# Kernel tuning notes

Hardware: AMD Instinct MI355X
Metric: run time of the kernel (lower is better)

## Reference

```python
import jax, jax.numpy as jnp
import numpy as np

B, H, W = 2, 32, 128
HW = H * W
N, C = 4096, 64
KQ, KN = 32, 16          # nsample_q, nsample
DIST = 10.0              # neighbor distance threshold
NEG = -1e10


def _knn(q, p, k):
    # q: (B,M,3), p: (B,N,3) -> idx (B,M,k), sqdist (B,M,k)
    sqd = jnp.sum((q[:, :, None, :] - p[:, None, :, :]) ** 2, axis=-1)
    neg, idx = jax.lax.top_k(-sqd, k)
    return idx, -neg


def _gather(p, idx):
    # p: (B,N,C), idx: (B,M,K) -> (B,M,K,C)
    return jax.vmap(lambda a, i: a[i])(p, idx)


def _norm_feat(x):
    # per-point channel normalization, torch.std default is unbiased (ddof=1)
    m = jnp.mean(x, axis=-1, keepdims=True)
    s = jnp.clip(jnp.std(x, axis=-1, keepdims=True, ddof=1), 1e-12)
    return (x - m) / s


def _conv(x, w, b, g, e):
    # 1x1 conv + BatchNorm (track_running_stats=False -> batch stats) + LeakyReLU(0.1)
    y = jnp.einsum('bnkc,cd->bnkd', x, w) + b
    mu = y.mean(axis=(0, 1, 2), keepdims=True)
    var = y.var(axis=(0, 1, 2), keepdims=True)
    y = (y - mu) * jax.lax.rsqrt(var + 1e-5) * g + e
    return jnp.where(y > 0, y, 0.1 * y)


def setup_inputs() -> dict:
    key = jax.random.key(0)
    ks = jax.random.split(key, 20)
    inp = {
        'xyz_proj_raw': jax.random.normal(ks[0], (B, H, W, 3), jnp.float32),
        'warped_xyz': jax.random.normal(ks[1], (B, HW, 3), jnp.float32),
        'warped_points': jax.random.normal(ks[2], (B, HW, C), jnp.float32),
        'idx_n2': jax.random.randint(ks[3], (B, HW, 2), 0, W),
        'f2_xyz': jax.random.normal(ks[4], (B, N, 3), jnp.float32),
        'f2_points': jax.random.normal(ks[5], (B, N, C), jnp.float32),
        'lidar_z': jax.random.uniform(ks[6], (B, HW, 1), jnp.float32),
    }
    shapes = {
        'm1w0': (70, 128), 'm1w1': (128, 64), 'piw': (6, 64),
        'm2w0': (128, 64), 'm2w1': (64, 64), 'pcw': (10, 64),
        'm3w0': (192, 64), 'm3w1': (64, 64),
    }
    i = 7
    for name, shp in shapes.items():
        inp[name] = jax.random.normal(ks[i], shp, jnp.float32) * 0.05
        i += 1
        pre = name[:-2] if name[-2] == 'w' else name[:-1]
        suf = name[-1] if name[-2] == 'w' else ''
        cout = shp[1]
        inp[pre + 'b' + suf] = jnp.zeros((cout,), jnp.float32)
        inp[pre + 'g' + suf] = jnp.ones((cout,), jnp.float32)
        inp[pre + 'e' + suf] = jnp.zeros((cout,), jnp.float32)
    return inp


def reference(xyz_proj_raw, warped_xyz, warped_points, idx_n2, f2_xyz, f2_points, lidar_z,
              m1w0, m1b0, m1g0, m1e0, m1w1, m1b1, m1g1, m1e1,
              piw, pib, pig, pie,
              m2w0, m2b0, m2g0, m2e0, m2w1, m2b1, m2g1, m2e1,
              pcw, pcb, pcg, pce,
              m3w0, m3b0, m3g0, m3e0, m3w1, m3b1, m3g1, m3e1):
    # ---- stage 1: cross kNN grouping into image features ----
    idx_q, _ = _knn(warped_xyz, f2_xyz, KQ)
    qi_xyz = _gather(f2_xyz, idx_q)          # (B,HW,KQ,3)
    qi_pts = _gather(f2_points, idx_q)       # (B,HW,KQ,C)

    wxyz = warped_xyz * lidar_z              # (B,HW,3)
    pi_xyz_exp = jnp.broadcast_to(wxyz[:, :, None, :], (B, HW, KQ, 3))
    pi_pts_exp = jnp.broadcast_to(warped_points[:, :, None, :], (B, HW, KQ, C))
    pi_xyz_diff_concat = jnp.concatenate([pi_xyz_exp, qi_xyz], axis=3)  # (B,HW,KQ,6)

    pi_feat_diff = _norm_feat(pi_pts_exp) * _norm_feat(qi_pts)          # correlation
    feat = jnp.concatenate([pi_xyz_diff_concat, pi_feat_diff], axis=3)  # (B,HW,KQ,70)

    feat = _conv(feat, m1w0, m1b0, m1g0, m1e0)
    feat = _conv(feat, m1w1, m1b1, m1g1, m1e1)                          # (B,HW,KQ,64)
    pi_enc = _conv(pi_xyz_diff_concat, piw, pib, pig, pie)              # (B,HW,KQ,64)

    pi_cat = jnp.concatenate([pi_enc, feat], axis=3)
    pi_cat = _conv(pi_cat, m2w0, m2b0, m2g0, m2e0)
    pi_cat = _conv(pi_cat, m2w1, m2b1, m2g1, m2e1)
    WQ = jax.nn.softmax(pi_cat, axis=2)
    pi_feat1 = jnp.sum(WQ * feat, axis=2)                               # (B,HW,64)

    # ---- stage 2: self kNN (use_trans=False -> raw projected xyz), thresholded validity ----
    xyz_pr = xyz_proj_raw.reshape(B, HW, 3)
    idx2, sqd2 = _knn(xyz_pr, xyz_pr, KN)
    valid = (sqd2 < DIST * DIST).astype(pi_feat1.dtype)[..., None]      # (B,HW,KN,1)

    pc_xyz_g = _gather(wxyz, idx2)                                      # (B,HW,KN,3)
    pc_pts_g = _gather(pi_feat1, idx2)                                  # (B,HW,KN,64)
    pc_xyz_new = jnp.broadcast_to(wxyz[:, :, None, :], (B, HW, KN, 3))
    pc_pts_new = jnp.broadcast_to(warped_points[:, :, None, :], (B, HW, KN, C))

    pc_diff = pc_xyz_g - pc_xyz_new
    pc_euc = jnp.sqrt(jnp.sum(pc_diff * pc_diff, axis=3, keepdims=True) + 1e-20)
    pc_xyz_cat = jnp.concatenate([pc_xyz_new, pc_xyz_g, pc_diff, pc_euc], axis=3)  # 10ch

    pc_enc = _conv(pc_xyz_cat, pcw, pcb, pcg, pce)
    pc_cat = jnp.concatenate([pc_enc, pc_pts_new, pc_pts_g], axis=-1)   # (B,HW,KN,192)
    pc_cat = _conv(pc_cat, m3w0, m3b0, m3g0, m3e0)
    pc_cat = _conv(pc_cat, m3w1, m3b1, m3g1, m3e1)

    pc_cat = pc_cat * valid + NEG * (1.0 - valid)
    WP = jax.nn.softmax(pc_cat, axis=2)
    out = jnp.sum(WP * pc_pts_g, axis=2)                                # (B,HW,64)
    return out.reshape(B, H, W, -1)
```

## Files before the change

### kernel.cpp

```cpp
#include <hip/hip_runtime.h>
#include <math.h>

constexpr int Bn  = 2;
constexpr int HWn = 4096;
constexpr int Nn  = 4096;
constexpr int KQn = 32;
constexpr int KNn = 16;
constexpr float INV_R1 = 1.0f/262144.0f;
constexpr float INV_R2 = 1.0f/131072.0f;

typedef _Float16 f16x8 __attribute__((ext_vector_type(8)));
typedef float    f32x4 __attribute__((ext_vector_type(4)));

__device__ __forceinline__ float wred64(float v){
  #pragma unroll
  for (int m = 32; m > 0; m >>= 1) v += __shfl_xor(v, m, 64);
  return v;
}
__device__ __forceinline__ float leakyf(float v){ return v > 0.f ? v : 0.1f*v; }

__device__ __forceinline__ void bn_param(const float* st, int c, float inv_n,
                                         const float* g, const float* e,
                                         float& sc, float& sh){
  float mu  = st[c]*inv_n;
  float var = st[128+c]*inv_n - mu*mu;
  float s   = g[c]*rsqrtf(var + 1e-5f);
  sc = s; sh = e[c] - mu*s;
}

__device__ __forceinline__ void build_x70(int row,
    const float* __restrict__ wxyz, const float* __restrict__ f2_xyz,
    const float* __restrict__ normW, const float* __restrict__ normF2,
    const int* __restrict__ idxq, float* x){
  int p = row >> 5;
  int b = p >> 12;
  int idx = idxq[row];
  const float* wx = wxyz + (size_t)p*3;
  const float* fx = f2_xyz + ((size_t)b*Nn + idx)*3;
  x[0]=wx[0]; x[1]=wx[1]; x[2]=wx[2];
  x[3]=fx[0]; x[4]=fx[1]; x[5]=fx[2];
  const float4* nw = (const float4*)(normW  + (size_t)p*64);
  const float4* nf = (const float4*)(normF2 + ((size_t)b*Nn + idx)*64);
  #pragma unroll
  for (int c=0;c<16;c++){
    float4 a = nw[c], q = nf[c];
    x[6+4*c+0]=a.x*q.x; x[6+4*c+1]=a.y*q.y; x[6+4*c+2]=a.z*q.z; x[6+4*c+3]=a.w*q.w;
  }
}

__device__ __forceinline__ void build_x10(int row,
    const float* __restrict__ wxyz, const int* __restrict__ idx2, float* x){
  int p = row >> 4, b = p >> 12;
  int idx = idx2[row];
  const float* nw = wxyz + (size_t)p*3;
  const float* gw = wxyz + ((size_t)b*HWn + idx)*3;
  float n0=nw[0],n1=nw[1],n2=nw[2];
  float g0=gw[0],g1=gw[1],g2=gw[2];
  float d0=g0-n0, d1=g1-n1, d2=g2-n2;
  x[0]=n0;x[1]=n1;x[2]=n2; x[3]=g0;x[4]=g1;x[5]=g2;
  x[6]=d0;x[7]=d1;x[8]=d2; x[9]=sqrtf(d0*d0+d1*d1+d2*d2+1e-20f);
}

__global__ __launch_bounds__(256) void k_prep(
    const float* __restrict__ warped_xyz, const float* __restrict__ lidar_z,
    const float* __restrict__ warped_points, const float* __restrict__ f2_points,
    const float* __restrict__ m1w0, const float* __restrict__ m1w1,
    const float* __restrict__ piw, const float* __restrict__ pcw,
    const float* __restrict__ m2w0, const float* __restrict__ m2w1,
    const float* __restrict__ m3w0, const float* __restrict__ m3w1,
    float* __restrict__ wxyz, float* __restrict__ normW, float* __restrict__ normF2,
    float* __restrict__ piwT, float* __restrict__ pcwT,
    _Float16* __restrict__ w1h, _Float16* __restrict__ w2h,
    _Float16* __restrict__ w3h, _Float16* __restrict__ w4h,
    _Float16* __restrict__ w5h, _Float16* __restrict__ w6h)
{
  int blk = blockIdx.x, tid = threadIdx.x;
  if (blk < 4096){
    int lane = tid & 63;
    int p = blk*4 + (tid >> 6);
    const float* src; float* dst;
    if (p < Bn*HWn){ src = warped_points + (size_t)p*64; dst = normW + (size_t)p*64; }
    else { int q = p - Bn*HWn; src = f2_points + (size_t)q*64; dst = normF2 + (size_t)q*64; }
    float x = src[lane];
    float m = wred64(x) * (1.f/64.f);
    float d = x - m;
    float ss = wred64(d*d);
    float s = fmaxf(sqrtf(ss*(1.f/63.f)), 1e-12f);
    dst[lane] = d / s;
  } else if (blk < 4192){
    int e = (blk-4096)*256 + tid;
    wxyz[e] = warped_xyz[e] * lidar_z[e/3];
  } else if (blk < 4196){
    int e = (blk-4192)*256 + tid;
    if (e < 384){ piwT[(e & 63)*6  + (e >> 6)] = piw[e]; }
    else if (e < 1024){ int f = e-384; pcwT[(f & 63)*10 + (f >> 6)] = pcw[f]; }
  } else {
    int e = (blk-4196)*256 + tid;
    if (e < 12288){
      int j = e/96, k = e - j*96;
      w1h[e] = (k < 70) ? (_Float16)m1w0[k*128 + j] : (_Float16)0.f;
    } else if (e < 20480){
      int f = e - 12288; int d = f >> 7, c = f & 127;
      w2h[f] = (_Float16)m1w1[c*64 + d];
    } else if (e < 28672){
      int f = e - 20480; int d = f >> 7, c = f & 127;
      w3h[f] = (_Float16)m2w0[c*64 + d];
    } else if (e < 32768){
      int f = e - 28672; int d = f >> 6, c = f & 63;
      w4h[f] = (_Float16)m2w1[c*64 + d];
    } else if (e < 45056){
      int f = e - 32768; int d = f/192, c = f - 192*d;
      w5h[f] = (_Float16)m3w0[c*64 + d];
    } else {
      int f = e - 45056; int d = f >> 6, c = f & 63;
      w6h[f] = (_Float16)m3w1[c*64 + d];
    }
  }
}

__global__ __launch_bounds__(256) void k_knn_all(
    const float* __restrict__ qA, const float* __restrict__ pA, int* __restrict__ oA,
    const float* __restrict__ qB, const float* __restrict__ pB, int* __restrict__ oB,
    float* __restrict__ ovalid)
{
  __shared__ int hist[4096];
  __shared__ int wsum[4];
  __shared__ unsigned int redm[4], redM[4];
  __shared__ int sh_sel, sh_rem, sh_cls, cnt_lt, cnt_eq;
  bool second = blockIdx.x >= 8192;
  int blk = second ? (blockIdx.x - 8192) : blockIdx.x;
  int K = second ? KNn : KQn;
  const float* qpts = second ? qB : qA;
  const float* pts  = second ? pB : pA;
  int* oidx = second ? oB : oA;
  int b = blk >> 12;
  int qi = blk & 4095;
  int tid = threadIdx.x;
  int lane = tid & 63, wv = tid >> 6;
  const float* qp = qpts + ((size_t)(b*HWn+qi))*3;
  float qx=qp[0], qy=qp[1], qz=qp[2];
  const float* pb = pts + (size_t)b*Nn*3;
  unsigned int key[16];
  {
    const float4* pb4 = (const float4*)(pb + (size_t)tid*48);
    float4 v[12];
    #pragma unroll
    for (int i=0;i<12;i++) v[i] = pb4[i];
    const float* f = (const float*)v;
    #pragma unroll
    for (int i=0;i<16;i++){
      float dx = __fsub_rn(qx, f[i*3+0]);
      float dy = __fsub_rn(qy, f[i*3+1]);
      float dz = __fsub_rn(qz, f[i*3+2]);
      float d2 = __fadd_rn(__fadd_rn(__fmul_rn(dx,dx), __fmul_rn(dy,dy)), __fmul_rn(dz,dz));
      key[i] = __float_as_uint(d2);
    }
  }
  unsigned int mn = key[0], mx = key[0];
  #pragma unroll
  for (int i=1;i<16;i++){ mn = min(mn, key[i]); mx = max(mx, key[i]); }
  #pragma unroll
  for (int m=32;m>0;m>>=1){
    mn = min(mn, (unsigned int)__shfl_xor((int)mn, m, 64));
    mx = max(mx, (unsigned int)__shfl_xor((int)mx, m, 64));
  }
  if (lane == 0){ redm[wv] = mn; redM[wv] = mx; }
  if (tid == 0){ cnt_lt = 0; cnt_eq = 0; }
  __syncthreads();
  mn = min(min(redm[0],redm[1]), min(redm[2],redm[3]));
  mx = max(max(redM[0],redM[1]), max(redM[2],redM[3]));
  unsigned int R = mx - mn;
  int L = (R == 0u) ? 0 : (31 - __clz(R));
  int shift = (L > 11) ? (L - 11) : 0;
  unsigned int dmask = 4095u;

  unsigned int active = 0xFFFFu, below = 0u;
  int rem = K;
  bool first = true;
  for (;;){
    __syncthreads();
    if (first){
      int4 z = {0,0,0,0};
      #pragma unroll
      for (int j=0;j<4;j++) ((int4*)hist)[tid + j*256] = z;
    } else {
      hist[tid] = 0;
    }
    __syncthreads();
    #pragma unroll
    for (int i=0;i<16;i++){
      if (active & (1u<<i))
        atomicAdd(&hist[(int)(((key[i]-mn) >> shift) & dmask)], 1);
    }
    __syncthreads();
    if (first){
      int base = tid*16;
      int hv[16]; int tot = 0;
      #pragma unroll
      for (int i=0;i<16;i++){ hv[i] = hist[base+i]; tot += hv[i]; }
      int pref = tot;
      #pragma unroll
      for (int m=1;m<64;m<<=1){ int t = __shfl_up(pref, m, 64); if (lane >= m) pref += t; }
      if (lane == 63) wsum[wv] = pref;
      __syncthreads();
      int off = 0;
      #pragma unroll
      for (int i=0;i<3;i++) if (i < wv) off += wsum[i];
      pref += off;
      if (pref >= rem && (pref - tot) < rem){
        int running = pref - tot;
        bool done = false;
        #pragma unroll
        for (int i=0;i<16;i++){
          if (!done && running + hv[i] >= rem){
            sh_sel = base + i;
            sh_rem = rem - running;
            sh_cls = hv[i];
            done = true;
          }
          if (!done) running += hv[i];
        }
      }
    } else {
      int h = hist[tid];
      int pref = h;
      #pragma unroll
      for (int m=1;m<64;m<<=1){ int t = __shfl_up(pref, m, 64); if (lane >= m) pref += t; }
      if (lane == 63) wsum[wv] = pref;
      __syncthreads();
      int off = 0;
      #pragma unroll
      for (int i=0;i<3;i++) if (i < wv) off += wsum[i];
      pref += off;
      if (pref >= rem && (pref - h) < rem){
        sh_sel = tid;
        sh_rem = rem - (pref - h);
        sh_cls = h;
      }
    }
    __syncthreads();
    unsigned int sel = (unsigned int)sh_sel; rem = sh_rem; int cls = sh_cls;
    #pragma unroll
    for (int i=0;i<16;i++){
      if (active & (1u<<i)){
        unsigned int d = ((key[i]-mn) >> shift) & dmask;
        if (d < sel) below |= (1u<<i);
        if (d != sel) active &= ~(1u<<i);
      }
    }
    if (cls == rem || shift == 0) break;
    int w = (shift < 8) ? shift : 8;
    shift -= w;
    dmask = (w == 8) ? 255u : ((1u<<w) - 1u);
    first = false;
  }
  size_t obase = ((size_t)(b*HWn+qi))*K;
  int nless = K - rem;
  const unsigned int U100 = __float_as_uint(100.0f);
  #pragma unroll
  for (int i=0;i<16;i++){
    if (below & (1u<<i)){
      int s = atomicAdd(&cnt_lt, 1);
      oidx[obase+s] = tid*16 + i;
      if (second) ovalid[obase+s] = (key[i] < U100) ? 1.f : 0.f;
    } else if (active & (1u<<i)){
      int s = atomicAdd(&cnt_eq, 1);
      if (s < rem){
        oidx[obase+nless+s] = tid*16 + i;
        if (second) ovalid[obase+nless+s] = (key[i] < U100) ? 1.f : 0.f;
      }
    }
  }
}

__global__ __launch_bounds__(256) void k_build_stats(
    const float* __restrict__ wxyz, const float* __restrict__ f2_xyz,
    const float* __restrict__ normW, const float* __restrict__ normF2,
    const int* __restrict__ idxq, const int* __restrict__ idx2,
    const _Float16* __restrict__ w1h,
    _Float16* __restrict__ X1, float* stats, float* __restrict__ gram)
{
  __shared__ float ssum[128], sssq[128];
  __shared__ float sacc[66];
  int blk = blockIdx.x, tid = threadIdx.x, lane = tid & 63;
  if (blk < 1024){
    int row = blk*256 + tid;
    {
      float x[70];
      build_x70(row, wxyz, f2_xyz, normW, normF2, idxq, x);
      unsigned int* d32 = (unsigned int*)(X1 + (size_t)row*96);
      union { unsigned int u; _Float16 h[2]; } pk;
      #pragma unroll
      for (int c=0;c<35;c++){
        pk.h[0] = (_Float16)x[2*c]; pk.h[1] = (_Float16)x[2*c+1];
        d32[c] = pk.u;
      }
      #pragma unroll
      for (int c=35;c<48;c++) d32[c] = 0u;
    }
    if (tid < 128){ ssum[tid]=0.f; sssq[tid]=0.f; }
    __syncthreads();
    int wave = tid >> 6;
    int quad = lane >> 4, n16 = lane & 15;
    float r1[8], r2[8];
    #pragma unroll
    for (int i=0;i<8;i++){ r1[i]=0.f; r2[i]=0.f; }
    for (int t=0;t<4;t++){
      int m0 = blk*256 + t*64 + wave*16;
      const _Float16* xr = X1 + (size_t)(m0 + n16)*96 + quad*8;
      f16x8 a0 = *(const f16x8*)(xr);
      f16x8 a1 = *(const f16x8*)(xr + 32);
      f16x8 a2 = *(const f16x8*)(xr + 64);
      #pragma unroll
      for (int nt = 0; nt < 8; nt++){
        const _Float16* wr = w1h + (size_t)(nt*16 + n16)*96 + quad*8;
        f16x8 b0 = *(const f16x8*)(wr);
        f16x8 b1 = *(const f16x8*)(wr + 32);
        f16x8 b2 = *(const f16x8*)(wr + 64);
        f32x4 acc = {0.f,0.f,0.f,0.f};
        acc = __builtin_amdgcn_mfma_f32_16x16x32_f16(a0, b0, acc, 0,0,0);
        acc = __builtin_amdgcn_mfma_f32_16x16x32_f16(a1, b1, acc, 0,0,0);
        acc = __builtin_amdgcn_mfma_f32_16x16x32_f16(a2, b2, acc, 0,0,0);
        float s1 = acc[0]+acc[1]+acc[2]+acc[3];
        float s2 = acc[0]*acc[0]+acc[1]*acc[1]+acc[2]*acc[2]+acc[3]*acc[3];
        s1 += __shfl_xor(s1, 16, 64); s1 += __shfl_xor(s1, 32, 64);
        s2 += __shfl_xor(s2, 16, 64); s2 += __shfl_xor(s2, 32, 64);
        r1[nt] += s1; r2[nt] += s2;
      }
    }
    if (quad == 0){
      #pragma unroll
      for (int nt=0;nt<8;nt++){
        atomicAdd(&ssum[nt*16+n16], r1[nt]); atomicAdd(&sssq[nt*16+n16], r2[nt]);
      }
    }
    __syncthreads();
    if (tid < 128){ atomicAdd(&stats[tid], ssum[tid]); atomicAdd(&stats[128+tid], sssq[tid]); }
  } else if (blk < 1088){
    float a[28];
    #pragma unroll
    for (int q=0;q<28;q++) a[q]=0.f;
    int g = (blk-1024)*256 + tid;
    for (int s=0;s<16;s++){
      int row = g + s*16384;
      int p = row >> 5, b = p >> 12;
      int idx = idxq[row];
      const float* wx = wxyz + (size_t)p*3;
      const float* fx = f2_xyz + ((size_t)b*Nn + idx)*3;
      float xt[7] = {wx[0],wx[1],wx[2],fx[0],fx[1],fx[2],1.f};
      int q=0;
      #pragma unroll
      for (int i=0;i<7;i++)
        #pragma unroll
        for (int j=i;j<7;j++) a[q++] += xt[i]*xt[j];
    }
    if (tid < 28) sacc[tid]=0.f;
    __syncthreads();
    #pragma unroll
    for (int q=0;q<28;q++){
      float v = wred64(a[q]);
      if (lane==0) atomicAdd(&sacc[q], v);
    }
    __syncthreads();
    if (tid < 28) atomicAdd(&gram[tid], sacc[tid]);
  } else {
    float a[66];
    #pragma unroll
    for (int q=0;q<66;q++) a[q]=0.f;
    int g = (blk-1088)*256 + tid;
    for (int s=0;s<16;s++){
      int row = g + s*8192;
      float x[10];
      build_x10(row, wxyz, idx2, x);
      float xt[11] = {x[0],x[1],x[2],x[3],x[4],x[5],x[6],x[7],x[8],x[9],1.f};
      int q=0;
      #pragma unroll
      for (int i=0;i<11;i++)
        #pragma unroll
        for (int j=i;j<11;j++) a[q++] += xt[i]*xt[j];
    }
    if (tid < 66) sacc[tid]=0.f;
    __syncthreads();
    #pragma unroll
    for (int q=0;q<66;q++){
      float v = wred64(a[q]);
      if (lane==0) atomicAdd(&sacc[q], v);
    }
    __syncthreads();
    if (tid < 66) atomicAdd(&gram[32+tid], sacc[tid]);
  }
}

__global__ __launch_bounds__(128) void k_gram_fin(
    const float* __restrict__ gram,
    const float* __restrict__ piw, const float* __restrict__ pib,
    const float* __restrict__ pcw, const float* __restrict__ pcb,
    float* stats)
{
  int tid = threadIdx.x;
  if (tid < 64){
    int c = tid;
    float wt[7];
    #pragma unroll
    for (int i=0;i<6;i++) wt[i] = piw[i*64+c];
    wt[6] = pib[c];
    const float* G = gram;
    float sum=0.f, ssq=0.f;
    #pragma unroll
    for (int i=0;i<7;i++){
      int offi = i*7 - (i*(i-1))/2;
      sum += wt[i]*G[offi + (6-i)];
      #pragma unroll
      for (int j=0;j<7;j++){
        int ii = i<j? i : j, jj = i<j? j : i;
        int o = ii*7 - (ii*(ii-1))/2 + (jj-ii);
        ssq += wt[i]*wt[j]*G[o];
      }
    }
    stats[2*256+c] = sum; stats[2*256+128+c] = ssq;
  } else {
    int c = tid-64;
    float wt[11];
    #pragma unroll
    for (int i=0;i<10;i++) wt[i] = pcw[i*64+c];
    wt[10] = pcb[c];
    const float* G = gram + 32;
    float sum=0.f, ssq=0.f;
    #pragma unroll
    for (int i=0;i<11;i++){
      int offi = i*11 - (i*(i-1))/2;
      sum += wt[i]*G[offi + (10-i)];
      #pragma unroll
      for (int j=0;j<11;j++){
        int ii = i<j? i : j, jj = i<j? j : i;
        int o = ii*11 - (ii*(ii-1))/2 + (jj-ii);
        ssq += wt[i]*wt[j]*G[o];
      }
    }
    stats[5*256+c] = sum; stats[5*256+128+c] = ssq;
  }
}

__global__ __launch_bounds__(256) void k_mfma_m1(
    const _Float16* __restrict__ X1, const _Float16* __restrict__ w1h,
    const _Float16* __restrict__ w2h,
    const float* __restrict__ m1g0, const float* __restrict__ m1e0,
    float* stats, _Float16* __restrict__ y2h)
{
  __shared__ _Float16 st[64*136];
  __shared__ float sc1[128], sh1[128], ssum[64], sssq[64];
  int tid = threadIdx.x;
  if (tid < 128){
    float s,h; bn_param(stats, tid, INV_R1, m1g0, m1e0, s, h);
    sc1[tid]=s; sh1[tid]=h;
  }
  if (tid < 64){ ssum[tid]=0.f; sssq[tid]=0.f; }
  __syncthreads();
  int wave = tid >> 6, lane = tid & 63;
  int quad = lane >> 4, n16 = lane & 15;
  float r1[4], r2[4];
  #pragma unroll
  for (int i=0;i<4;i++){ r1[i]=0.f; r2[i]=0.f; }
  for (int t=0;t<4;t++){
    int m0 = blockIdx.x*256 + t*64 + wave*16;
    const _Float16* xr = X1 + (size_t)(m0 + n16)*96 + quad*8;
    f16x8 a0 = *(const f16x8*)(xr);
    f16x8 a1 = *(const f16x8*)(xr + 32);
    f16x8 a2 = *(const f16x8*)(xr + 64);
    #pragma unroll
    for (int nt = 0; nt < 8; nt++){
      const _Float16* wr = w1h + (size_t)(nt*16 + n16)*96 + quad*8;
      f16x8 b0 = *(const f16x8*)(wr);
      f16x8 b1 = *(const f16x8*)(wr + 32);
      f16x8 b2 = *(const f16x8*)(wr + 64);
      f32x4 acc = {0.f,0.f,0.f,0.f};
      acc = __builtin_amdgcn_mfma_f32_16x16x32_f16(a0, b0, acc, 0,0,0);
      acc = __builtin_amdgcn_mfma_f32_16x16x32_f16(a1, b1, acc, 0,0,0);
      acc = __builtin_amdgcn_mfma_f32_16x16x32_f16(a2, b2, acc, 0,0,0);
      int ch = nt*16 + n16;
      float sc = sc1[ch], sh = sh1[ch];
      #pragma unroll
      for (int r=0;r<4;r++){
        float v = leakyf(acc[r]*sc + sh);
        st[(size_t)(wave*16 + quad*4 + r)*136 + ch] = (_Float16)v;
      }
    }
    __syncthreads();
    const _Float16* tr = st + (size_t)(wave*16 + n16)*136 + quad*8;
    f16x8 t0 = *(const f16x8*)(tr);
    f16x8 t1 = *(const f16x8*)(tr + 32);
    f16x8 t2 = *(const f16x8*)(tr + 64);
    f16x8 t3 = *(const f16x8*)(tr + 96);
    #pragma unroll
    for (int nt = 0; nt < 4; nt++){
      const _Float16* wr = w2h + (size_t)(nt*16 + n16)*128 + quad*8;
      f16x8 b0 = *(const f16x8*)(wr);
      f16x8 b1 = *(const f16x8*)(wr + 32);
      f16x8 b2 = *(const f16x8*)(wr + 64);
      f16x8 b3 = *(const f16x8*)(wr + 96);
      f32x4 acc = {0.f,0.f,0.f,0.f};
      acc = __builtin_amdgcn_mfma_f32_16x16x32_f16(t0, b0, acc, 0,0,0);
      acc = __builtin_amdgcn_mfma_f32_16x16x32_f16(t1, b1, acc, 0,0,0);
      acc = __builtin_amdgcn_mfma_f32_16x16x32_f16(t2, b2, acc, 0,0,0);
      acc = __builtin_amdgcn_mfma_f32_16x16x32_f16(t3, b3, acc, 0,0,0);
      int ch = nt*16 + n16;
      #pragma unroll
      for (int r=0;r<4;r++){
        int rowg = blockIdx.x*256 + t*64 + wave*16 + quad*4 + r;
        y2h[(size_t)rowg*64 + ch] = (_Float16)acc[r];
      }
      float s1 = acc[0]+acc[1]+acc[2]+acc[3];
      float s2 = acc[0]*acc[0]+acc[1]*acc[1]+acc[2]*acc[2]+acc[3]*acc[3];
      s1 += __shfl_xor(s1, 16, 64); s1 += __shfl_xor(s1, 32, 64);
      s2 += __shfl_xor(s2, 16, 64); s2 += __shfl_xor(s2, 32, 64);
      r1[nt] += s1; r2[nt] += s2;
    }
    __syncthreads();
  }
  if (quad == 0){
    #pragma unroll
    for (int nt=0;nt<4;nt++){
      atomicAdd(&ssum[nt*16+n16], r1[nt]); atomicAdd(&sssq[nt*16+n16], r2[nt]);
    }
  }
  __syncthreads();
  if (tid < 64){ atomicAdd(&stats[1*256+tid], ssum[tid]); atomicAdd(&stats[1*256+128+tid], sssq[tid]); }
}

__global__ __launch_bounds__(256) void k_mfma_m2a(
    const float* __restrict__ wxyz, const float* __restrict__ f2_xyz,
    const int* __restrict__ idxq,
    const float* __restrict__ piwT, const float* __restrict__ pib,
    const float* __restrict__ pig, const float* __restrict__ pie,
    const float* __restrict__ m1g1, const float* __restrict__ m1e1,
    const _Float16* __restrict__ y2h, const _Float16* __restrict__ w3h,
    float* stats, _Float16* __restrict__ y3h)
{
  __shared__ _Float16 su[64*136];
  __shared__ float spw[384];
  __shared__ float scp[64], shp[64], sc2[64], sh2[64], ssum[64], sssq[64];
  int tid = threadIdx.x;
  for (int d = tid; d < 384; d += 256) spw[d] = piwT[d];
  if (tid < 64){
    float s,h;
    bn_param(stats+2*256, tid, INV_R1, pig,  pie,  s, h); scp[tid]=s; shp[tid]=h;
    bn_param(stats+1*256, tid, INV_R1, m1g1, m1e1, s, h); sc2[tid]=s; sh2[tid]=h;
    ssum[tid]=0.f; sssq[tid]=0.f;
  }
  __syncthreads();
  int r = tid & 63, cg = tid >> 6;
  int wave = tid >> 6, lane = tid & 63, quad = lane >> 4, n16 = lane & 15;
  float r1[4], r2[4];
  #pragma unroll
  for (int i=0;i<4;i++){ r1[i]=0.f; r2[i]=0.f; }
  for (int t=0;t<4;t++){
    int rowg = blockIdx.x*256 + t*64 + r;
    {
      int p = rowg >> 5, b = p >> 12;
      int idx = idxq[rowg];
      const float* wx = wxyz + (size_t)p*3;
      const float* fx = f2_xyz + ((size_t)b*Nn + idx)*3;
      float x0=wx[0],x1=wx[1],x2=wx[2],x3=fx[0],x4=fx[1],x5=fx[2];
      #pragma unroll
      for (int jj=0;jj<16;jj++){
        int j = cg*16 + jj;
        const float* pw = spw + j*6;
        float e = pib[j] + x0*pw[0]+x1*pw[1]+x2*pw[2]+x3*pw[3]+x4*pw[4]+x5*pw[5];
        su[r*136 + j] = (_Float16)leakyf(e*scp[j] + shp[j]);
      }
      const f16x8* yr = (const f16x8*)(y2h + (size_t)rowg*64 + cg*16);
      f16x8 q0 = yr[0], q1 = yr[1];
      #pragma unroll
      for (int jj=0;jj<8;jj++){
        int c = cg*16 + jj;
        su[r*136 + 64 + c] = (_Float16)leakyf((float)q0[jj]*sc2[c] + sh2[c]);
      }
      #pragma unroll
      for (int jj=0;jj<8;jj++){
        int c = cg*16 + 8 + jj;
        su[r*136 + 64 + c] = (_Float16)leakyf((float)q1[jj]*sc2[c] + sh2[c]);
      }
    }
    __syncthreads();
    const _Float16* ur = su + (size_t)(wave*16 + n16)*136 + quad*8;
    f16x8 a0 = *(const f16x8*)(ur);
    f16x8 a1 = *(const f16x8*)(ur + 32);
    f16x8 a2 = *(const f16x8*)(ur + 64);
    f16x8 a3 = *(const f16x8*)(ur + 96);
    #pragma unroll
    for (int nt = 0; nt < 4; nt++){
      const _Float16* wr = w3h + (size_t)(nt*16 + n16)*128 + quad*8;
      f16x8 b0 = *(const f16x8*)(wr);
      f16x8 b1 = *(const f16x8*)(wr + 32);
      f16x8 b2 = *(const f16x8*)(wr + 64);
      f16x8 b3 = *(const f16x8*)(wr + 96);
      f32x4 acc = {0.f,0.f,0.f,0.f};
      acc = __builtin_amdgcn_mfma_f32_16x16x32_f16(a0, b0, acc, 0,0,0);
      acc = __builtin_amdgcn_mfma_f32_16x16x32_f16(a1, b1, acc, 0,0,0);
      acc = __builtin_amdgcn_mfma_f32_16x16x32_f16(a2, b2, acc, 0,0,0);
      acc = __builtin_amdgcn_mfma_f32_16x16x32_f16(a3, b3, acc, 0,0,0);
      int ch = nt*16 + n16;
      #pragma unroll
      for (int rr=0;rr<4;rr++){
        int rg = blockIdx.x*256 + t*64 + wave*16 + quad*4 + rr;
        y3h[(size_t)rg*64 + ch] = (_Float16)acc[rr];
      }
      float s1 = acc[0]+acc[1]+acc[2]+acc[3];
      float s2 = acc[0]*acc[0]+acc[1]*acc[1]+acc[2]*acc[2]+acc[3]*acc[3];
      s1 += __shfl_xor(s1, 16, 64); s1 += __shfl_xor(s1, 32, 64);
      s2 += __shfl_xor(s2, 16, 64); s2 += __shfl_xor(s2, 32, 64);
      r1[nt] += s1; r2[nt] += s2;
    }
    __syncthreads();
  }
  if (quad == 0){
    #pragma unroll
    for (int nt=0;nt<4;nt++){
      atomicAdd(&ssum[nt*16+n16], r1[nt]); atomicAdd(&sssq[nt*16+n16], r2[nt]);
    }
  }
  __syncthreads();
  if (tid < 64){ atomicAdd(&stats[3*256+tid], ssum[tid]); atomicAdd(&stats[3*256+128+tid], sssq[tid]); }
}

__global__ __launch_bounds__(256) void k_mfma_pw64(
    const _Float16* __restrict__ yin, const _Float16* __restrict__ wh,
    const float* __restrict__ g, const float* __restrict__ e,
    const float* statsIn, float* statsOut, float inv_n,
    _Float16* __restrict__ yout)
{
  __shared__ _Float16 stt[64*72];
  __shared__ float sc[64], sh[64], ssum[64], sssq[64];
  int tid = threadIdx.x;
  if (tid < 64){
    float s,h; bn_param(statsIn, tid, inv_n, g, e, s, h);
    sc[tid]=s; sh[tid]=h; ssum[tid]=0.f; sssq[tid]=0.f;
  }
  __syncthreads();
  int r = tid & 63, cg = tid >> 6;
  int wave = tid >> 6, lane = tid & 63, quad = lane >> 4, n16 = lane & 15;
  float r1[4], r2[4];
  #pragma unroll
  for (int i=0;i<4;i++){ r1[i]=0.f; r2[i]=0.f; }
  for (int t=0;t<4;t++){
    int rowg = blockIdx.x*256 + t*64 + r;
    const f16x8* yr = (const f16x8*)(yin + (size_t)rowg*64 + cg*16);
    f16x8 q0 = yr[0], q1 = yr[1];
    #pragma unroll
    for (int jj=0;jj<8;jj++){
      int c = cg*16 + jj;
      stt[r*72 + c] = (_Float16)leakyf((float)q0[jj]*sc[c] + sh[c]);
    }
    #pragma unroll
    for (int jj=0;jj<8;jj++){
      int c = cg*16 + 8 + jj;
      stt[r*72 + c] = (_Float16)leakyf((float)q1[jj]*sc[c] + sh[c]);
    }
    __syncthreads();
    const _Float16* tr = stt + (size_t)(wave*16 + n16)*72 + quad*8;
    f16x8 a0 = *(const f16x8*)(tr);
    f16x8 a1 = *(const f16x8*)(tr + 32);
    #pragma unroll
    for (int nt = 0; nt < 4; nt++){
      const _Float16* wr = wh + (size_t)(nt*16 + n16)*64 + quad*8;
      f16x8 b0 = *(const f16x8*)(wr);
      f16x8 b1 = *(const f16x8*)(wr + 32);
      f32x4 acc = {0.f,0.f,0.f,0.f};
      acc = __builtin_amdgcn_mfma_f32_16x16x32_f16(a0, b0, acc, 0,0,0);
      acc = __builtin_amdgcn_mfma_f32_16x16x32_f16(a1, b1, acc, 0,0,0);
      int ch = nt*16 + n16;
      #pragma unroll
      for (int rr=0;rr<4;rr++){
        int rg = blockIdx.x*256 + t*64 + wave*16 + quad*4 + rr;
        yout[(size_t)rg*64 + ch] = (_Float16)acc[rr];
      }
      float s1 = acc[0]+acc[1]+acc[2]+acc[3];
      float s2 = acc[0]*acc[0]+acc[1]*acc[1]+acc[2]*acc[2]+acc[3]*acc[3];
      s1 += __shfl_xor(s1, 16, 64); s1 += __shfl_xor(s1, 32, 64);
      s2 += __shfl_xor(s2, 16, 64); s2 += __shfl_xor(s2, 32, 64);
      r1[nt] += s1; r2[nt] += s2;
    }
    __syncthreads();
  }
  if (quad == 0){
    #pragma unroll
    for (int nt=0;nt<4;nt++){
      atomicAdd(&ssum[nt*16+n16], r1[nt]); atomicAdd(&sssq[nt*16+n16], r2[nt]);
    }
  }
  __syncthreads();
  if (tid < 64){ atomicAdd(&statsOut[tid], ssum[tid]); atomicAdd(&statsOut[128+tid], sssq[tid]); }
}

__global__ __launch_bounds__(256) void k_mfma_m3a(
    const float* __restrict__ wxyz, const float* __restrict__ warped_points,
    const _Float16* __restrict__ pif1h, const int* __restrict__ idx2,
    const float* __restrict__ pcwT, const float* __restrict__ pcb,
    const float* __restrict__ pcg, const float* __restrict__ pce,
    const _Float16* __restrict__ w5h,
    float* stats, _Float16* __restrict__ y5h)
{
  __shared__ _Float16 sv[64*200];
  __shared__ float spw[640];
  __shared__ float scp[64], shp[64], ssum[64], sssq[64];
  int tid = threadIdx.x;
  for (int d = tid; d < 640; d += 256) spw[d] = pcwT[d];
  if (tid < 64){
    float s,h; bn_param(stats+5*256, tid, INV_R2, pcg, pce, s, h);
    scp[tid]=s; shp[tid]=h; ssum[tid]=0.f; sssq[tid]=0.f;
  }
  __syncthreads();
  int r = tid & 63, cg = tid >> 6;
  int wave = tid >> 6, lane = tid & 63, quad = lane >> 4, n16 = lane & 15;
  float r1[4], r2[4];
  #pragma unroll
  for (int i=0;i<4;i++){ r1[i]=0.f; r2[i]=0.f; }
  for (int t=0;t<4;t++){
    int rowg = blockIdx.x*256 + t*64 + r;
    {
      int p = rowg >> 4, b = p >> 12;
      int idx = idx2[rowg];
      float x[10];
      build_x10(rowg, wxyz, idx2, x);
      #pragma unroll
      for (int jj=0;jj<16;jj++){
        int j = cg*16 + jj;
        const float* pw = spw + j*10;
        float e = pcb[j];
        #pragma unroll
        for (int i=0;i<10;i++) e += x[i]*pw[i];
        sv[r*200 + j] = (_Float16)leakyf(e*scp[j] + shp[j]);
      }
      const float4* wp = (const float4*)(warped_points + (size_t)p*64 + cg*16);
      #pragma unroll
      for (int v4=0; v4<4; v4++){
        float4 q = wp[v4];
        int c = 64 + cg*16 + v4*4;
        sv[r*200 + c + 0] = (_Float16)q.x;
        sv[r*200 + c + 1] = (_Float16)q.y;
        sv[r*200 + c + 2] = (_Float16)q.z;
        sv[r*200 + c + 3] = (_Float16)q.w;
      }
      const f16x8* pg = (const f16x8*)(pif1h + ((size_t)(b*HWn) + idx)*64 + cg*16);
      f16x8 g0 = pg[0], g1 = pg[1];
      #pragma unroll
      for (int jj=0;jj<8;jj++) sv[r*200 + 128 + cg*16 + jj] = g0[jj];
      #pragma unroll
      for (int jj=0;jj<8;jj++) sv[r*200 + 136 + cg*16 + jj] = g1[jj];
    }
    __syncthreads();
    const _Float16* vr = sv + (size_t)(wave*16 + n16)*200 + quad*8;
    f16x8 a0 = *(const f16x8*)(vr);
    f16x8 a1 = *(const f16x8*)(vr + 32);
    f16x8 a2 = *(const f16x8*)(vr + 64);
    f16x8 a3 = *(const f16x8*)(vr + 96);
    f16x8 a4 = *(const f16x8*)(vr + 128);
    f16x8 a5 = *(const f16x8*)(vr + 160);
    #pragma unroll
    for (int nt = 0; nt < 4; nt++){
      const _Float16* wr = w5h + (size_t)(nt*16 + n16)*192 + quad*8;
      f32x4 acc = {0.f,0.f,0.f,0.f};
      acc = __builtin_amdgcn_mfma_f32_16x16x32_f16(a0, *(const f16x8*)(wr),       acc, 0,0,0);
      acc = __builtin_amdgcn_mfma_f32_16x16x32_f16(a1, *(const f16x8*)(wr + 32),  acc, 0,0,0);
      acc = __builtin_amdgcn_mfma_f32_16x16x32_f16(a2, *(const f16x8*)(wr + 64),  acc, 0,0,0);
      acc = __builtin_amdgcn_mfma_f32_16x16x32_f16(a3, *(const f16x8*)(wr + 96),  acc, 0,0,0);
      acc = __builtin_amdgcn_mfma_f32_16x16x32_f16(a4, *(const f16x8*)(wr + 128), acc, 0,0,0);
      acc = __builtin_amdgcn_mfma_f32_16x16x32_f16(a5, *(const f16x8*)(wr + 160), acc, 0,0,0);
      int ch = nt*16 + n16;
      #pragma unroll
      for (int rr=0;rr<4;rr++){
        int rg = blockIdx.x*256 + t*64 + wave*16 + quad*4 + rr;
        y5h[(size_t)rg*64 + ch] = (_Float16)acc[rr];
      }
      float s1 = acc[0]+acc[1]+acc[2]+acc[3];
      float s2 = acc[0]*acc[0]+acc[1]*acc[1]+acc[2]*acc[2]+acc[3]*acc[3];
      s1 += __shfl_xor(s1, 16, 64); s1 += __shfl_xor(s1, 32, 64);
      s2 += __shfl_xor(s2, 16, 64); s2 += __shfl_xor(s2, 32, 64);
      r1[nt] += s1; r2[nt] += s2;
    }
    __syncthreads();
  }
  if (quad == 0){
    #pragma unroll
    for (int nt=0;nt<4;nt++){
      atomicAdd(&ssum[nt*16+n16], r1[nt]); atomicAdd(&sssq[nt*16+n16], r2[nt]);
    }
  }
  __syncthreads();
  if (tid < 64){ atomicAdd(&stats[6*256+tid], ssum[tid]); atomicAdd(&stats[6*256+128+tid], sssq[tid]); }
}

__global__ __launch_bounds__(256) void k_softmax1(
    const _Float16* __restrict__ y2h, const _Float16* __restrict__ y4h,
    const float* stats,
    const float* __restrict__ m1g1, const float* __restrict__ m1e1,
    const float* __restrict__ m2g1, const float* __restrict__ m2e1,
    _Float16* __restrict__ pif1h)
{
  int tid = threadIdx.x, lane = tid & 63;
  int p = blockIdx.x*4 + (tid >> 6);
  int d = lane;
  float sc2,sh2,sc4,sh4;
  bn_param(stats+1*256, d, INV_R1, m1g1, m1e1, sc2, sh2);
  bn_param(stats+4*256, d, INV_R1, m2g1, m2e1, sc4, sh4);
  size_t rb = (size_t)p*KQn;
  float v[32]; float mx = -1e30f;
  #pragma unroll
  for (int k=0;k<32;k++){
    float t = leakyf((float)y4h[(rb+k)*64 + d]*sc4 + sh4);
    v[k] = t; mx = fmaxf(mx, t);
  }
  float se = 0.f;
  #pragma unroll
  for (int k=0;k<32;k++){ float ev = __expf(v[k]-mx); v[k]=ev; se += ev; }
  float inv = 1.f/se, acc = 0.f;
  #pragma unroll
  for (int k=0;k<32;k++){
    float f = leakyf((float)y2h[(rb+k)*64 + d]*sc2 + sh2);
    acc += v[k]*f;
  }
  pif1h[(size_t)p*64 + d] = (_Float16)(acc*inv);
}

__global__ __launch_bounds__(256) void k_softmax2(
    const _Float16* __restrict__ y6h, const _Float16* __restrict__ pif1h,
    const int* __restrict__ idx2, const float* __restrict__ validf,
    const float* stats,
    const float* __restrict__ m3g1, const float* __restrict__ m3e1,
    float* __restrict__ out)
{
  int tid = threadIdx.x, lane = tid & 63;
  int p = blockIdx.x*4 + (tid >> 6);
  int b = p >> 12;
  int d = lane;
  float sc,sh; bn_param(stats+7*256, d, INV_R2, m3g1, m3e1, sc, sh);
  size_t rb = (size_t)p*KNn;
  float v[16]; float mx = -1e30f;
  #pragma unroll
  for (int k=0;k<16;k++){
    float t = leakyf((float)y6h[(rb+k)*64 + d]*sc + sh);
    t = (validf[rb+k] > 0.5f) ? t : -1e10f;
    v[k] = t; mx = fmaxf(mx, t);
  }
  float se = 0.f;
  #pragma unroll
  for (int k=0;k<16;k++){ float ev = __expf(v[k]-mx); v[k]=ev; se += ev; }
  float inv = 1.f/se, acc = 0.f;
  #pragma unroll
  for (int k=0;k<16;k++){
    int idx = idx2[rb+k];
    acc += v[k]*(float)pif1h[((size_t)(b*HWn) + idx)*64 + d];
  }
  out[(size_t)p*64 + d] = acc*inv;
}

extern "C" void kernel_launch(void* const* d_in, const int* in_sizes, int n_in,
                              void* d_out, int out_size, void* d_ws, size_t ws_size,
                              hipStream_t stream)
{
  (void)in_sizes; (void)n_in; (void)out_size; (void)ws_size;
  const float* xyz_proj      = (const float*)d_in[0];
  const float* warped_xyz    = (const float*)d_in[1];
  const float* warped_points = (const float*)d_in[2];
  const float* f2_xyz        = (const float*)d_in[4];
  const float* f2_points     = (const float*)d_in[5];
  const float* lidar_z       = (const float*)d_in[6];
  const float* m1w0=(const float*)d_in[7],  *m1g0=(const float*)d_in[9],  *m1e0=(const float*)d_in[10];
  const float* m1w1=(const float*)d_in[11], *m1g1=(const float*)d_in[13], *m1e1=(const float*)d_in[14];
  const float* piw =(const float*)d_in[15], *pib =(const float*)d_in[16], *pig =(const float*)d_in[17], *pie =(const float*)d_in[18];
  const float* m2w0=(const float*)d_in[19], *m2g0=(const float*)d_in[21], *m2e0=(const float*)d_in[22];
  const float* m2w1=(const float*)d_in[23], *m2g1=(const float*)d_in[25], *m2e1=(const float*)d_in[26];
  const float* pcw =(const float*)d_in[27], *pcb =(const float*)d_in[28], *pcg =(const float*)d_in[29], *pce =(const float*)d_in[30];
  const float* m3w0=(const float*)d_in[31], *m3g0=(const float*)d_in[33], *m3e0=(const float*)d_in[34];
  const float* m3w1=(const float*)d_in[35], *m3g1=(const float*)d_in[37], *m3e1=(const float*)d_in[38];
  float* out = (float*)d_out;

  float* ws     = (float*)d_ws;
  float* wxyz   = ws;
  float* normW  = wxyz   + 24576;
  float* normF2 = normW  + 524288;
  float* piwT   = normF2 + 524288;
  float* pcwT   = piwT   + 384;
  float* stats  = pcwT   + 640;
  float* gram   = stats  + 2048;
  int*   idxq   = (int*)(gram + 128);
  int*   idx2   = idxq   + 262144;
  float* validf = (float*)(idx2 + 131072);
  _Float16* pif1h = (_Float16*)(validf + 131072);
  float* X1f    = validf + 131072 + 524288;
  _Float16* X1  = (_Float16*)X1f;
  float* y2f    = X1f + 12582912;
  _Float16* y2h = (_Float16*)y2f;
  float* y3f    = y2f + 8388608;
  _Float16* y3h = (_Float16*)y3f;
  float* whb    = y3f + 8388608;
  _Float16* w1h = (_Float16*)whb;
  _Float16* w2h = w1h + 12288;
  _Float16* w3h = w2h + 8192;
  _Float16* w4h = w3h + 8192;
  _Float16* w5h = w4h + 4096;
  _Float16* w6h = w5h + 12288;
  _Float16* y4h = (_Float16*)X1f;
  _Float16* y5h = (_Float16*)(X1f + 8388608);
  _Float16* y6h = y3h;

  hipMemsetAsync(stats, 0, (2048+128)*sizeof(float), stream);
  k_prep<<<4388,256,0,stream>>>(warped_xyz, lidar_z, warped_points, f2_points,
                                m1w0, m1w1, piw, pcw, m2w0, m2w1, m3w0, m3w1,
                                wxyz, normW, normF2, piwT, pcwT,
                                w1h, w2h, w3h, w4h, w5h, w6h);
  k_knn_all<<<16384,256,0,stream>>>(warped_xyz, f2_xyz, idxq,
                                    xyz_proj, xyz_proj, idx2, validf);
  k_build_stats<<<1120,256,0,stream>>>(wxyz, f2_xyz, normW, normF2, idxq, idx2,
                                       w1h, X1, stats, gram);
  k_gram_fin<<<1,128,0,stream>>>(gram, piw, pib, pcw, pcb, stats);
  k_mfma_m1<<<1024,256,0,stream>>>(X1, w1h, w2h, m1g0, m1e0, stats, y2h);
  k_mfma_m2a<<<1024,256,0,stream>>>(wxyz, f2_xyz, idxq, piwT, pib, pig, pie,
                                    m1g1, m1e1, y2h, w3h, stats, y3h);
  k_mfma_pw64<<<1024,256,0,stream>>>(y3h, w4h, m2g0, m2e0,
                                     stats+3*256, stats+4*256, INV_R1, y4h);
  k_softmax1<<<2048,256,0,stream>>>(y2h, y4h, stats, m1g1, m1e1, m2g1, m2e1, pif1h);
  k_mfma_m3a<<<512,256,0,stream>>>(wxyz, warped_points, pif1h, idx2,
                                   pcwT, pcb, pcg, pce, w5h, stats, y5h);
  k_mfma_pw64<<<512,256,0,stream>>>(y5h, w6h, m3g0, m3e0,
                                    stats+6*256, stats+7*256, INV_R2, y6h);
  k_softmax2<<<2048,256,0,stream>>>(y6h, pif1h, idx2, validf, stats, m3g1, m3e1, out);
}
```

Baseline: 525.7 us.

## Replace iterative radix-select with single histogram pass plus boundary-bucket rank sort

The top-k radix select now builds only one 4096-bin histogram and stops. Ties in the boundary bucket are resolved by copying those candidates into shared memory, where one wavefront ranks them exactly by key and index. Histogram slots are also permuted so that each thread's 16 bins sit at a stride of 256, which should reduce LDS bank conflicts during the prefix read. This removes the multiple refinement passes and their barriers. The trade-off is an O(cls^2) rank loop on a single wave when the boundary bucket is large, and boundary buckets beyond 2048 entries would be truncated.

Result: faster. 504.1 us (-4.1%).

```diff
diff --git a/kernel.cpp b/kernel.cpp
--- a/kernel.cpp
+++ b/kernel.cpp
@@ -156,6 +156,11 @@
       key[i] = __float_as_uint(d2);
     }
   }
+  {
+    int4 z = {0,0,0,0};
+    #pragma unroll
+    for (int j=0;j<4;j++) ((int4*)hist)[tid + j*256] = z;
+  }
   unsigned int mn = key[0], mx = key[0];
   #pragma unroll
   for (int i=1;i<16;i++){ mn = min(mn, key[i]); mx = max(mx, key[i]); }
@@ -172,102 +177,73 @@
   unsigned int R = mx - mn;
   int L = (R == 0u) ? 0 : (31 - __clz(R));
   int shift = (L > 11) ? (L - 11) : 0;
-  unsigned int dmask = 4095u;
-
-  unsigned int active = 0xFFFFu, below = 0u;
-  int rem = K;
-  bool first = true;
-  for (;;){
-    __syncthreads();
-    if (first){
-      int4 z = {0,0,0,0};
-      #pragma unroll
-      for (int j=0;j<4;j++) ((int4*)hist)[tid + j*256] = z;
-    } else {
-      hist[tid] = 0;
-    }
-    __syncthreads();
-    #pragma unroll
-    for (int i=0;i<16;i++){
-      if (active & (1u<<i))
-        atomicAdd(&hist[(int)(((key[i]-mn) >> shift) & dmask)], 1);
-    }
-    __syncthreads();
-    if (first){
-      int base = tid*16;
-      int hv[16]; int tot = 0;
-      #pragma unroll
-      for (int i=0;i<16;i++){ hv[i] = hist[base+i]; tot += hv[i]; }
-      int pref = tot;
-      #pragma unroll
-      for (int m=1;m<64;m<<=1){ int t = __shfl_up(pref, m, 64); if (lane >= m) pref += t; }
-      if (lane == 63) wsum[wv] = pref;
-      __syncthreads();
-      int off = 0;
-      #pragma unroll
-      for (int i=0;i<3;i++) if (i < wv) off += wsum[i];
-      pref += off;
-      if (pref >= rem && (pref - tot) < rem){
-        int running = pref - tot;
-        bool done = false;
-        #pragma unroll
-        for (int i=0;i<16;i++){
-          if (!done && running + hv[i] >= rem){
-            sh_sel = base + i;
-            sh_rem = rem - running;
-            sh_cls = hv[i];
-            done = true;
-          }
-          if (!done) running += hv[i];
+  #pragma unroll
+  for (int i=0;i<16;i++){
+    unsigned int d = ((key[i]-mn) >> shift) & 4095u;
+    int slot = (int)(((d & 15u) << 8) | (d >> 4));
+    atomicAdd(&hist[slot], 1);
+  }
+  __syncthreads();
+  {
+    int hv[16]; int tot = 0;
+    #pragma unroll
+    for (int i=0;i<16;i++){ hv[i] = hist[tid + i*256]; tot += hv[i]; }
+    int pref = tot;
+    #pragma unroll
+    for (int m=1;m<64;m<<=1){ int t = __shfl_up(pref, m, 64); if (lane >= m) pref += t; }
+    if (lane == 63) wsum[wv] = pref;
+    __syncthreads();
+    int off = 0;
+    #pragma unroll
+    for (int i=0;i<3;i++) if (i < wv) off += wsum[i];
+    pref += off;
+    if (pref >= K && (pref - tot) < K){
+      int running = pref - tot;
+      bool done = false;
+      #pragma unroll
+      for (int i=0;i<16;i++){
+        if (!done && running + hv[i] >= K){
+          sh_sel = tid*16 + i;
+          sh_rem = K - running;
+          sh_cls = hv[i];
+          done = true;
         }
-      }
-    } else {
-      int h = hist[tid];
-      int pref = h;
-      #pragma unroll
-      for (int m=1;m<64;m<<=1){ int t = __shfl_up(pref, m, 64); if (lane >= m) pref += t; }
-      if (lane == 63) wsum[wv] = pref;
-      __syncthreads();
-      int off = 0;
-      #pragma unroll
-      for (int i=0;i<3;i++) if (i < wv) off += wsum[i];
-      pref += off;
-      if (pref >= rem && (pref - h) < rem){
-        sh_sel = tid;
-        sh_rem = rem - (pref - h);
-        sh_cls = h;
-      }
-    }
-    __syncthreads();
-    unsigned int sel = (unsigned int)sh_sel; rem = sh_rem; int cls = sh_cls;
-    #pragma unroll
-    for (int i=0;i<16;i++){
-      if (active & (1u<<i)){
-        unsigned int d = ((key[i]-mn) >> shift) & dmask;
-        if (d < sel) below |= (1u<<i);
-        if (d != sel) active &= ~(1u<<i);
-      }
-    }
-    if (cls == rem || shift == 0) break;
-    int w = (shift < 8) ? shift : 8;
-    shift -= w;
-    dmask = (w == 8) ? 255u : ((1u<<w) - 1u);
-    first = false;
-  }
+        if (!done) running += hv[i];
+      }
+    }
+  }
+  __syncthreads();
+  unsigned int sel = (unsigned int)sh_sel;
+  int rem = sh_rem, cls = sh_cls;
+  int nless = K - rem;
   size_t obase = ((size_t)(b*HWn+qi))*K;
-  int nless = K - rem;
   const unsigned int U100 = __float_as_uint(100.0f);
   #pragma unroll
   for (int i=0;i<16;i++){
-    if (below & (1u<<i)){
+    unsigned int d = ((key[i]-mn) >> shift) & 4095u;
+    if (d < sel){
       int s = atomicAdd(&cnt_lt, 1);
       oidx[obase+s] = tid*16 + i;
       if (second) ovalid[obase+s] = (key[i] < U100) ? 1.f : 0.f;
-    } else if (active & (1u<<i)){
+    } else if (d == sel){
       int s = atomicAdd(&cnt_eq, 1);
-      if (s < rem){
-        oidx[obase+nless+s] = tid*16 + i;
-        if (second) ovalid[obase+nless+s] = (key[i] < U100) ? 1.f : 0.f;
+      if (s < 2048){ hist[s] = (int)key[i]; hist[2048+s] = tid*16 + i; }
+    }
+  }
+  __syncthreads();
+  if (wv == 0){
+    int cc = cls < 2048 ? cls : 2048;
+    for (int c = lane; c < cc; c += 64){
+      unsigned int kc = (unsigned int)hist[c];
+      int ic = hist[2048+c];
+      int rank = 0;
+      for (int j = 0; j < cc; j++){
+        unsigned int kj = (unsigned int)hist[j];
+        if (kj < kc || (kj == kc && hist[2048+j] < ic)) rank++;
+      }
+      if (rank < rem){
+        oidx[obase + nless + rank] = ic;
+        if (second) ovalid[obase + nless + rank] = (kc < U100) ? 1.f : 0.f;
       }
     }
   }
```
